# Kernel optimization log

Measured on AMD Instinct MI355X. Metric: run time of the kernel, lower is better.

Reference implementation:

```python
import jax, jax.numpy as jnp
import numpy as np

H_DIM = 1024
N_HEADS = 16
HEAD_D = H_DIM // N_HEADS  # 64


def setup_inputs() -> dict:
    key = jax.random.key(0)
    ks = jax.random.split(key, 10)
    B, T, C = 2, 2048, H_DIM
    init = 1.0 / np.sqrt(C)  # lecun_normal-scale stand-in
    src = jax.random.normal(ks[0], (B, T, C), dtype=jnp.float32)
    mask = jnp.ones((B, T), dtype=jnp.float32)  # unused when causal
    Wq = jax.random.normal(ks[1], (C, H_DIM), dtype=jnp.float32) * init
    Wk = jax.random.normal(ks[2], (C, H_DIM), dtype=jnp.float32) * init
    Wv = jax.random.normal(ks[3], (C, H_DIM), dtype=jnp.float32) * init
    Wo = jax.random.normal(ks[4], (H_DIM, H_DIM), dtype=jnp.float32) * init
    bq = jnp.zeros((H_DIM,), jnp.float32)
    bk = jnp.zeros((H_DIM,), jnp.float32)
    bv = jnp.zeros((H_DIM,), jnp.float32)
    bo = jnp.zeros((H_DIM,), jnp.float32)
    return {"src": src, "mask": mask, "Wq": Wq, "bq": bq, "Wk": Wk, "bk": bk,
            "Wv": Wv, "bv": bv, "Wo": Wo, "bo": bo}


def reference(src, mask, Wq, bq, Wk, bk, Wv, bv, Wo, bo):
    # MaskedCausalAttention forward, deterministic=True (dropout = identity),
    # use_causal_mask=True.
    B, T, C = src.shape
    N, D = N_HEADS, HEAD_D
    # q,k,v: [B, N, T, D]
    q = (src @ Wq + bq).reshape(B, T, N, D).transpose(0, 2, 1, 3)
    k = (src @ Wk + bk).reshape(B, T, N, D).transpose(0, 2, 1, 3)
    v = (src @ Wv + bv).reshape(B, T, N, D).transpose(0, 2, 1, 3)
    # scores: [B, N, T, T]
    scores = jnp.einsum('bntd,bnsd->bnts', q, k) / jnp.sqrt(jnp.float32(D))
    causal = jnp.tril(jnp.ones((T, T), dtype=bool))[None, None]
    scores = jnp.where(causal, scores, -jnp.inf)
    probs = jax.nn.softmax(scores, axis=-1)
    attn = jnp.einsum('bnts,bnsd->bntd', probs, v)  # [B, N, T, D]
    attn = attn.transpose(0, 2, 1, 3).reshape(B, T, N * D)
    return attn @ Wo + bo
```

## Files before the change

kernel.cpp:

```cpp
#include <hip/hip_runtime.h>
#include <hip/hip_bf16.h>

typedef __hip_bfloat16 bf16;
typedef __attribute__((ext_vector_type(8))) short short8;
typedef __attribute__((ext_vector_type(4))) float f32x4;

#define BATCH 2
#define SEQ   2048
#define HDIM  1024
#define NHEAD 16
#define DHEAD 64
#define MROWS (BATCH*SEQ)

#define QSCALE 0.18033688f
#define EXP2F(x) __builtin_amdgcn_exp2f(x)

static __device__ __forceinline__ short f2bs(float x) {
    __hip_bfloat16 h = (__hip_bfloat16)x;
    return *reinterpret_cast<short*>(&h);
}
static __device__ __forceinline__ unsigned int pk2(float a, float b) {
    __hip_bfloat162 h = __float22bfloat162_rn(make_float2(a, b));
    return *reinterpret_cast<unsigned int*>(&h);
}

static __device__ __forceinline__ void gload16(const void* g, void* l) {
    __builtin_amdgcn_global_load_lds(
        (const __attribute__((address_space(1))) unsigned int*)g,
        (__attribute__((address_space(3))) unsigned int*)l, 16, 0, 0);
}

__global__ __launch_bounds__(256) void prep1(const float* __restrict__ src,
        const float* __restrict__ Wq, const float* __restrict__ Wk,
        const float* __restrict__ Wv, const float* __restrict__ Wo,
        short* __restrict__ Sb, short* __restrict__ WT,
        short* __restrict__ WoT)
{
    __shared__ float t[64][65];
    const int bx = blockIdx.x, tid = threadIdx.x;
    if (bx < 4096) {
        int i = bx * 256 + tid;
        float4 v = ((const float4*)src)[i];
        ushort4 o;
        o.x = (unsigned short)f2bs(v.x);
        o.y = (unsigned short)f2bs(v.y);
        o.z = (unsigned short)f2bs(v.z);
        o.w = (unsigned short)f2bs(v.w);
        ((ushort4*)Sb)[i] = o;
        return;
    }
    const int tb = bx - 4096;
    const int wsel = tb >> 8;
    const float* W = (wsel == 0) ? Wq : (wsel == 1) ? Wk : (wsel == 2) ? Wv : Wo;
    short* dst = (wsel < 3) ? WT : WoT;
    const int roff = (wsel < 3) ? wsel * 1024 : 0;
    const int t8 = tb & 255;
    const int n0 = (t8 & 15) * 64, k0 = (t8 >> 4) * 64;
#pragma unroll
    for (int i = 0; i < 16; i++) {
        int idx = tid + i * 256, r = idx >> 6, c = idx & 63;
        t[r][c] = W[(size_t)(k0 + r) * HDIM + n0 + c];
    }
    __syncthreads();
#pragma unroll
    for (int i = 0; i < 16; i++) {
        int idx = tid + i * 256, c = idx >> 6, r = idx & 63;
        dst[(size_t)(roff + n0 + c) * HDIM + k0 + r] = f2bs(t[r][c]);
    }
}

__global__ __launch_bounds__(256) void gemm_qkv(const short* __restrict__ A,
        const short* __restrict__ Bt,
        const float* __restrict__ bq, const float* __restrict__ bk,
        const float* __restrict__ bv,
        short* __restrict__ Qout, short* __restrict__ Kout,
        short* __restrict__ Vtout)
{
    __shared__ short As[16 * 512];
    __shared__ short Bs[16 * 512];
    const int tid = threadIdx.x, lane = tid & 63, w = tid >> 6;
    const int quad = lane >> 4, l15 = lane & 15;
    const int m0 = blockIdx.y * 128, n0 = blockIdx.x * 128;
    const int wr = w >> 1, wc = w & 1;

    const short* gsrc[8];
    short* ldst[8];
#pragma unroll
    for (int i = 0; i < 8; i++) {
        int u = w * 8 + i;
        if (u < 16) {
            int mi = u >> 1, kh = u & 1;
            gsrc[i] = A + (size_t)(m0 + mi * 16 + l15) * HDIM + kh * 32 + quad * 8;
            ldst[i] = &As[u * 512];
        } else {
            int v = u - 16, ni = v >> 1, kh = v & 1;
            gsrc[i] = Bt + (size_t)(n0 + ni * 16 + l15) * HDIM + kh * 32 + quad * 8;
            ldst[i] = &Bs[v * 512];
        }
    }

    f32x4 acc[4][4];
#pragma unroll
    for (int i = 0; i < 4; i++)
#pragma unroll
        for (int j = 0; j < 4; j++) acc[i][j] = (f32x4){0.f, 0.f, 0.f, 0.f};

    for (int kk = 0; kk < 16; ++kk) {
        if (kk) __syncthreads();
#pragma unroll
        for (int i = 0; i < 8; i++) {
            gload16(gsrc[i], ldst[i]);
            gsrc[i] += 64;
        }
        __syncthreads();

#pragma unroll
        for (int kh = 0; kh < 2; kh++) {
            short8 af[4], bfr[4];
#pragma unroll
            for (int mi = 0; mi < 4; mi++)
                af[mi] = *(const short8*)&As[((wr * 4 + mi) * 2 + kh) * 512 + lane * 8];
#pragma unroll
            for (int ni = 0; ni < 4; ni++)
                bfr[ni] = *(const short8*)&Bs[((wc * 4 + ni) * 2 + kh) * 512 + lane * 8];
#pragma unroll
            for (int mi = 0; mi < 4; mi++)
#pragma unroll
                for (int ni = 0; ni < 4; ni++)
                    acc[mi][ni] = __builtin_amdgcn_mfma_f32_16x16x32_bf16(
                                      af[mi], bfr[ni], acc[mi][ni], 0, 0, 0);
        }
    }

    const int region = n0 >> 10;
    if (region < 2) {
        const float* bias = region ? bk : bq;
        const float oscale = region ? 1.0f : QSCALE;
        short* C = region ? Kout : Qout;
#pragma unroll
        for (int mi = 0; mi < 4; mi++) {
            int mB = m0 + (wr * 4 + mi) * 16 + quad * 4;
#pragma unroll
            for (int ni = 0; ni < 4; ni++) {
                int nl = (n0 + (wc * 4 + ni) * 16 + l15) & 1023;
                float bb = bias[nl];
#pragma unroll
                for (int r = 0; r < 4; r++)
                    C[(size_t)(mB + r) * HDIM + nl] =
                        f2bs((acc[mi][ni][r] + bb) * oscale);
            }
        }
    } else {
#pragma unroll
        for (int mi = 0; mi < 4; mi++) {
            int mB = m0 + (wr * 4 + mi) * 16 + quad * 4;
            int bb = mB >> 11, t = mB & 2047;
#pragma unroll
            for (int ni = 0; ni < 4; ni++) {
                int n = n0 + (wc * 4 + ni) * 16 + l15;
                int h = (n >> 6) & 15, d = n & 63;
                float bvv = bv[n & 1023];
                size_t base = ((size_t)((bb * NHEAD + h) * DHEAD + d)) * SEQ + t;
                ushort4 pk;
                pk.x = (unsigned short)f2bs(acc[mi][ni][0] + bvv);
                pk.y = (unsigned short)f2bs(acc[mi][ni][1] + bvv);
                pk.z = (unsigned short)f2bs(acc[mi][ni][2] + bvv);
                pk.w = (unsigned short)f2bs(acc[mi][ni][3] + bvv);
                *(ushort4*)(Vtout + base) = pk;
            }
        }
    }
}

__global__ __launch_bounds__(256) void attn_mfma(const short* __restrict__ Qb,
        const short* __restrict__ Kb, const short* __restrict__ Vt,
        short* __restrict__ Ab)
{
    __shared__ short SMEM[20992];
    const int tid = threadIdx.x, lane = tid & 63, w = tid >> 6;
    const int quad = lane >> 4, l15 = lane & 15;
    const int L = blockIdx.x;

    const int pair = (L & 7) + 8 * ((L >> 3) & 3);
    const int strip = 31 - (L >> 5);
    const int b = pair >> 4, head = pair & 15;

    const short* Kbh = Kb + (size_t)b * SEQ * HDIM + head * DHEAD;
    const short* Vth = Vt + (size_t)(b * NHEAD + head) * DHEAD * SEQ;
    short* Pw = SMEM + 16384 + w * 1152;

    const int qbase = strip * 64;
    const int qr = qbase + w * 16 + l15;

    const short* qptr = Qb + (size_t)(b * SEQ + qr) * HDIM + head * DHEAD + quad * 8;
    short8 bq0 = *(const short8*)qptr;
    short8 bq1 = *(const short8*)(qptr + 32);

    const short* gp[4];
    int stp[4], ldo[4];
#pragma unroll
    for (int i = 0; i < 4; i++) {
        int u = w * 4 + i;
        if (u < 8) {
            int t = u >> 1, h = u & 1;
            gp[i] = Kbh + (size_t)(t * 16 + l15) * HDIM + h * 32 + quad * 8;
            stp[i] = 64 * HDIM;
        } else {
            int c = u - 8, dt = c >> 1, kh = c & 1;
            gp[i] = Vth + (size_t)(dt * 16 + l15) * SEQ + kh * 32 + quad * 8;
            stp[i] = 64;
        }
        ldo[i] = u * 512;
    }

    f32x4 o[4];
#pragma unroll
    for (int dt = 0; dt < 4; dt++) o[dt] = (f32x4){0.f, 0.f, 0.f, 0.f};
    float psum = 0.f;

#pragma unroll
    for (int i = 0; i < 4; i++) { gload16(gp[i], &SMEM[ldo[i]]); gp[i] += stp[i]; }

    for (int it = 0; it <= strip; ++it) {
        const int cur = it & 1;
        short* Ks = &SMEM[cur * 8192];
        short* Vs = Ks + 4096;

        if (it < strip) {
            short* nb = &SMEM[(cur ^ 1) * 8192];
#pragma unroll
            for (int i = 0; i < 4; i++) { gload16(gp[i], nb + ldo[i]); gp[i] += stp[i]; }
            asm volatile("s_waitcnt vmcnt(4)" ::: "memory");
        } else {
            asm volatile("s_waitcnt vmcnt(0)" ::: "memory");
        }
        __builtin_amdgcn_s_barrier();
        const int s0 = it * 64;
        f32x4 sv[4];
        __builtin_amdgcn_s_setprio(1);
#pragma unroll
        for (int t = 0; t < 4; t++) {
            sv[t] = (f32x4){0.f, 0.f, 0.f, 0.f};
            short8 k0 = *(const short8*)&Ks[(t * 2) * 512 + lane * 8];
            short8 k1 = *(const short8*)&Ks[(t * 2 + 1) * 512 + lane * 8];
            sv[t] = __builtin_amdgcn_mfma_f32_16x16x32_bf16(k0, bq0, sv[t], 0, 0, 0);
            sv[t] = __builtin_amdgcn_mfma_f32_16x16x32_bf16(k1, bq1, sv[t], 0, 0, 0);
        }
        __builtin_amdgcn_s_setprio(0);

        float p[16];
        if (it == strip) {
#pragma unroll
            for (int t = 0; t < 4; t++)
#pragma unroll
                for (int r = 0; r < 4; r++) {
                    int key = s0 + t * 16 + quad * 4 + r;
                    p[t * 4 + r] = (key <= qr) ? EXP2F(sv[t][r]) : 0.f;
                }
        } else {
#pragma unroll
            for (int t = 0; t < 4; t++)
#pragma unroll
                for (int r = 0; r < 4; r++)
                    p[t * 4 + r] = EXP2F(sv[t][r]);
        }
#pragma unroll
        for (int i = 0; i < 16; i++) psum += p[i];

#pragma unroll
        for (int t = 0; t < 4; t++) {
            uint2 u2;
            u2.x = pk2(p[t * 4],     p[t * 4 + 1]);
            u2.y = pk2(p[t * 4 + 2], p[t * 4 + 3]);
            *(uint2*)&Pw[l15 * 72 + t * 16 + quad * 4] = u2;
        }
        short8 bp0 = *(const short8*)&Pw[l15 * 72 + quad * 8];
        short8 bp1 = *(const short8*)&Pw[l15 * 72 + 32 + quad * 8];

        __builtin_amdgcn_s_setprio(1);
#pragma unroll
        for (int dt = 0; dt < 4; dt++) {
            short8 av0 = *(const short8*)&Vs[(dt * 2) * 512 + lane * 8];
            short8 av1 = *(const short8*)&Vs[(dt * 2 + 1) * 512 + lane * 8];
            o[dt] = __builtin_amdgcn_mfma_f32_16x16x32_bf16(av0, bp0, o[dt], 0, 0, 0);
            o[dt] = __builtin_amdgcn_mfma_f32_16x16x32_bf16(av1, bp1, o[dt], 0, 0, 0);
        }
        __builtin_amdgcn_s_setprio(0);
        __builtin_amdgcn_s_barrier();
    }

    float lrow = psum + __shfl_xor(psum, 16);
    lrow += __shfl_xor(lrow, 32);
    const float inv = 1.f / lrow;

    const size_t obase = (size_t)(b * SEQ + qr) * HDIM + head * DHEAD;
#pragma unroll
    for (int dt = 0; dt < 4; dt++) {
        uint2 u2;
        u2.x = pk2(o[dt][0] * inv, o[dt][1] * inv);
        u2.y = pk2(o[dt][2] * inv, o[dt][3] * inv);
        *(uint2*)&Ab[obase + dt * 16 + quad * 4] = u2;
    }
}

__global__ __launch_bounds__(256) void gemm_o(const short* __restrict__ A,
        const short* __restrict__ Bt, const float* __restrict__ bo,
        float* __restrict__ Out)
{
    __shared__ short As[8 * 512];
    __shared__ short Bs[16 * 512];
    const int tid = threadIdx.x, lane = tid & 63, w = tid >> 6;
    const int quad = lane >> 4, l15 = lane & 15;
    const int m0 = blockIdx.y * 64, n0 = blockIdx.x * 128;
    const int wr = w >> 1, wc = w & 1;

    const short* gsrc[6];
    short* ldst[6];
#pragma unroll
    for (int i = 0; i < 6; i++) {
        int u = w * 6 + i;
        if (u < 8) {
            int mi = u >> 1, kh = u & 1;
            gsrc[i] = A + (size_t)(m0 + mi * 16 + l15) * HDIM + kh * 32 + quad * 8;
            ldst[i] = &As[u * 512];
        } else {
            int v = u - 8, ni = v >> 1, kh = v & 1;
            gsrc[i] = Bt + (size_t)(n0 + ni * 16 + l15) * HDIM + kh * 32 + quad * 8;
            ldst[i] = &Bs[v * 512];
        }
    }

    f32x4 acc[2][4];
#pragma unroll
    for (int i = 0; i < 2; i++)
#pragma unroll
        for (int j = 0; j < 4; j++) acc[i][j] = (f32x4){0.f, 0.f, 0.f, 0.f};

    for (int kk = 0; kk < 16; ++kk) {
        if (kk) __syncthreads();
#pragma unroll
        for (int i = 0; i < 6; i++) {
            gload16(gsrc[i], ldst[i]);
            gsrc[i] += 64;
        }
        __syncthreads();

#pragma unroll
        for (int kh = 0; kh < 2; kh++) {
            short8 af[2], bfr[4];
#pragma unroll
            for (int mi = 0; mi < 2; mi++)
                af[mi] = *(const short8*)&As[((wr * 2 + mi) * 2 + kh) * 512 + lane * 8];
#pragma unroll
            for (int ni = 0; ni < 4; ni++)
                bfr[ni] = *(const short8*)&Bs[((wc * 4 + ni) * 2 + kh) * 512 + lane * 8];
#pragma unroll
            for (int mi = 0; mi < 2; mi++)
#pragma unroll
                for (int ni = 0; ni < 4; ni++)
                    acc[mi][ni] = __builtin_amdgcn_mfma_f32_16x16x32_bf16(
                                      af[mi], bfr[ni], acc[mi][ni], 0, 0, 0);
        }
    }

#pragma unroll
    for (int mi = 0; mi < 2; mi++) {
        int mB = m0 + (wr * 2 + mi) * 16 + quad * 4;
#pragma unroll
        for (int ni = 0; ni < 4; ni++) {
            int n = n0 + (wc * 4 + ni) * 16 + l15;
            float bb = bo[n];
#pragma unroll
            for (int r = 0; r < 4; r++)
                Out[(size_t)(mB + r) * HDIM + n] = acc[mi][ni][r] + bb;
        }
    }
}

extern "C" void kernel_launch(void* const* d_in, const int* in_sizes, int n_in,
                              void* d_out, int out_size, void* d_ws, size_t ws_size,
                              hipStream_t stream)
{
    const float* src = (const float*)d_in[0];
    const float* Wq = (const float*)d_in[2];
    const float* bq = (const float*)d_in[3];
    const float* Wk = (const float*)d_in[4];
    const float* bk = (const float*)d_in[5];
    const float* Wv = (const float*)d_in[6];
    const float* bv = (const float*)d_in[7];
    const float* Wo = (const float*)d_in[8];
    const float* bo = (const float*)d_in[9];
    float* out = (float*)d_out;

    short* Sb   = (short*)d_ws;
    short* Qb   = Sb + (size_t)MROWS * HDIM;
    short* Kb   = Qb + (size_t)MROWS * HDIM;
    short* Vt   = Kb + (size_t)MROWS * HDIM;
    short* WoT  = Vt + (size_t)MROWS * HDIM;
    short* WT   = (short*)d_out;
    short* Ab   = Qb;

    dim3 blk(256);

    prep1<<<dim3(4096 + 1024), blk, 0, stream>>>(src, Wq, Wk, Wv, Wo, Sb, WT, WoT);

    gemm_qkv<<<dim3(24, 32), blk, 0, stream>>>(Sb, WT, bq, bk, bv, Qb, Kb, Vt);

    attn_mfma<<<dim3(1024), blk, 0, stream>>>(Qb, Kb, Vt, Ab);

    gemm_o<<<dim3(8, 64), blk, 0, stream>>>(Ab, WoT, bo, out);
}
```

Before: 224.7 us.

## Double-buffer LDS tiles in QKV and output GEMMs with async prefetch

Both GEMM kernels now keep two LDS stages and issue the global-to-LDS loads for the next k-tile before computing on the current one. Explicit vmcnt waits and raw s_barrier calls replace the two __syncthreads per iteration, so load latency can overlap the MFMA work. This doubles LDS use per block, which may lower occupancy. Correctness relies on the hand-written waitcnt values matching the outstanding load count and on the barrier not waiting for LDS reads.

Measured after the change: 210.8 us. 6.2% less time.

```diff
diff --git a/kernel.cpp b/kernel.cpp
--- a/kernel.cpp
+++ b/kernel.cpp
@@ -76,8 +76,7 @@
         short* __restrict__ Qout, short* __restrict__ Kout,
         short* __restrict__ Vtout)
 {
-    __shared__ short As[16 * 512];
-    __shared__ short Bs[16 * 512];
+    __shared__ short SM[2 * 16384];
     const int tid = threadIdx.x, lane = tid & 63, w = tid >> 6;
     const int quad = lane >> 4, l15 = lane & 15;
     const int m0 = blockIdx.y * 128, n0 = blockIdx.x * 128;
@@ -91,11 +90,11 @@
         if (u < 16) {
             int mi = u >> 1, kh = u & 1;
             gsrc[i] = A + (size_t)(m0 + mi * 16 + l15) * HDIM + kh * 32 + quad * 8;
-            ldst[i] = &As[u * 512];
+            ldst[i] = &SM[u * 512];
         } else {
             int v = u - 16, ni = v >> 1, kh = v & 1;
             gsrc[i] = Bt + (size_t)(n0 + ni * 16 + l15) * HDIM + kh * 32 + quad * 8;
-            ldst[i] = &Bs[v * 512];
+            ldst[i] = &SM[8192 + v * 512];
         }
     }
 
@@ -105,24 +104,31 @@
 #pragma unroll
         for (int j = 0; j < 4; j++) acc[i][j] = (f32x4){0.f, 0.f, 0.f, 0.f};
 
+#pragma unroll
+    for (int i = 0; i < 8; i++) { gload16(gsrc[i], ldst[i]); gsrc[i] += 64; }
+
     for (int kk = 0; kk < 16; ++kk) {
-        if (kk) __syncthreads();
-#pragma unroll
-        for (int i = 0; i < 8; i++) {
-            gload16(gsrc[i], ldst[i]);
-            gsrc[i] += 64;
-        }
-        __syncthreads();
-
+        const int cur = kk & 1;
+        if (kk < 15) {
+            const int nb = (cur ^ 1) << 14;
+#pragma unroll
+            for (int i = 0; i < 8; i++) { gload16(gsrc[i], ldst[i] + nb); gsrc[i] += 64; }
+            asm volatile("s_waitcnt vmcnt(8)" ::: "memory");
+        } else {
+            asm volatile("s_waitcnt vmcnt(0)" ::: "memory");
+        }
+        __builtin_amdgcn_s_barrier();
+        const short* Asb = &SM[cur << 14];
+        const short* Bsb = Asb + 8192;
 #pragma unroll
         for (int kh = 0; kh < 2; kh++) {
             short8 af[4], bfr[4];
 #pragma unroll
             for (int mi = 0; mi < 4; mi++)
-                af[mi] = *(const short8*)&As[((wr * 4 + mi) * 2 + kh) * 512 + lane * 8];
+                af[mi] = *(const short8*)&Asb[((wr * 4 + mi) * 2 + kh) * 512 + lane * 8];
 #pragma unroll
             for (int ni = 0; ni < 4; ni++)
-                bfr[ni] = *(const short8*)&Bs[((wc * 4 + ni) * 2 + kh) * 512 + lane * 8];
+                bfr[ni] = *(const short8*)&Bsb[((wc * 4 + ni) * 2 + kh) * 512 + lane * 8];
 #pragma unroll
             for (int mi = 0; mi < 4; mi++)
 #pragma unroll
@@ -130,6 +136,7 @@
                     acc[mi][ni] = __builtin_amdgcn_mfma_f32_16x16x32_bf16(
                                       af[mi], bfr[ni], acc[mi][ni], 0, 0, 0);
         }
+        __builtin_amdgcn_s_barrier();
     }
 
     const int region = n0 >> 10;
@@ -307,8 +314,7 @@
         const short* __restrict__ Bt, const float* __restrict__ bo,
         float* __restrict__ Out)
 {
-    __shared__ short As[8 * 512];
-    __shared__ short Bs[16 * 512];
+    __shared__ short SM[2 * 12288];
     const int tid = threadIdx.x, lane = tid & 63, w = tid >> 6;
     const int quad = lane >> 4, l15 = lane & 15;
     const int m0 = blockIdx.y * 64, n0 = blockIdx.x * 128;
@@ -322,11 +328,11 @@
         if (u < 8) {
             int mi = u >> 1, kh = u & 1;
             gsrc[i] = A + (size_t)(m0 + mi * 16 + l15) * HDIM + kh * 32 + quad * 8;
-            ldst[i] = &As[u * 512];
+            ldst[i] = &SM[u * 512];
         } else {
             int v = u - 8, ni = v >> 1, kh = v & 1;
             gsrc[i] = Bt + (size_t)(n0 + ni * 16 + l15) * HDIM + kh * 32 + quad * 8;
-            ldst[i] = &Bs[v * 512];
+            ldst[i] = &SM[4096 + v * 512];
         }
     }
 
@@ -336,24 +342,32 @@
 #pragma unroll
         for (int j = 0; j < 4; j++) acc[i][j] = (f32x4){0.f, 0.f, 0.f, 0.f};
 
+#pragma unroll
+    for (int i = 0; i < 6; i++) { gload16(gsrc[i], ldst[i]); gsrc[i] += 64; }
+
     for (int kk = 0; kk < 16; ++kk) {
-        if (kk) __syncthreads();
-#pragma unroll
-        for (int i = 0; i < 6; i++) {
-            gload16(gsrc[i], ldst[i]);
-            gsrc[i] += 64;
-        }
-        __syncthreads();
-
+        const int cur = kk & 1;
+        if (kk < 15) {
+            const int nb = (cur ^ 1) * 12288;
+#pragma unroll
+            for (int i = 0; i < 6; i++) { gload16(gsrc[i], ldst[i] + nb); gsrc[i] += 64; }
+            asm volatile("s_waitcnt vmcnt(6)" ::: "memory");
+        } else {
+            asm volatile("s_waitcnt vmcnt(0)" ::: "memory");
+        }
+        __builtin_amdgcn_s_barrier();
+
+        const short* Asb = &SM[cur * 12288];
+        const short* Bsb = Asb + 4096;
 #pragma unroll
         for (int kh = 0; kh < 2; kh++) {
             short8 af[2], bfr[4];
 #pragma unroll
             for (int mi = 0; mi < 2; mi++)
-                af[mi] = *(const short8*)&As[((wr * 2 + mi) * 2 + kh) * 512 + lane * 8];
+                af[mi] = *(const short8*)&Asb[((wr * 2 + mi) * 2 + kh) * 512 + lane * 8];
 #pragma unroll
             for (int ni = 0; ni < 4; ni++)
-                bfr[ni] = *(const short8*)&Bs[((wc * 4 + ni) * 2 + kh) * 512 + lane * 8];
+                bfr[ni] = *(const short8*)&Bsb[((wc * 4 + ni) * 2 + kh) * 512 + lane * 8];
 #pragma unroll
             for (int mi = 0; mi < 2; mi++)
 #pragma unroll
@@ -361,6 +375,7 @@
                     acc[mi][ni] = __builtin_amdgcn_mfma_f32_16x16x32_bf16(
                                       af[mi], bfr[ni], acc[mi][ni], 0, 0, 0);
         }
+        __builtin_amdgcn_s_barrier();
     }
 
 #pragma unroll
```

## Load GEMM fragments directly from global memory into registers with double buffering

Applied to the files above, without the earlier changes.

Both projection GEMMs stop staging tiles in LDS with global-to-LDS loads and barriers. Each wave now loads its MFMA A/B fragments straight from global memory into registers, using a two-stage register double buffer to overlap loads with MFMAs, and the launch bounds ask for two blocks per CU. This removes LDS traffic and __syncthreads, but tiles shared between waves are now loaded redundantly from global/L2, and the 16-byte row-strided fragment loads are less coalesced.

New measurement: 296.3 us. +31.9%, slower.

```diff
diff --git a/kernel.cpp b/kernel.cpp
--- a/kernel.cpp
+++ b/kernel.cpp
@@ -69,35 +69,26 @@
     }
 }
 
-__global__ __launch_bounds__(256) void gemm_qkv(const short* __restrict__ A,
+__global__ __launch_bounds__(256, 2) void gemm_qkv(const short* __restrict__ A,
         const short* __restrict__ Bt,
         const float* __restrict__ bq, const float* __restrict__ bk,
         const float* __restrict__ bv,
         short* __restrict__ Qout, short* __restrict__ Kout,
         short* __restrict__ Vtout)
 {
-    __shared__ short As[16 * 512];
-    __shared__ short Bs[16 * 512];
     const int tid = threadIdx.x, lane = tid & 63, w = tid >> 6;
     const int quad = lane >> 4, l15 = lane & 15;
     const int m0 = blockIdx.y * 128, n0 = blockIdx.x * 128;
     const int wr = w >> 1, wc = w & 1;
 
-    const short* gsrc[8];
-    short* ldst[8];
-#pragma unroll
-    for (int i = 0; i < 8; i++) {
-        int u = w * 8 + i;
-        if (u < 16) {
-            int mi = u >> 1, kh = u & 1;
-            gsrc[i] = A + (size_t)(m0 + mi * 16 + l15) * HDIM + kh * 32 + quad * 8;
-            ldst[i] = &As[u * 512];
-        } else {
-            int v = u - 16, ni = v >> 1, kh = v & 1;
-            gsrc[i] = Bt + (size_t)(n0 + ni * 16 + l15) * HDIM + kh * 32 + quad * 8;
-            ldst[i] = &Bs[v * 512];
-        }
-    }
+    const short* ap[4];
+    const short* bp[4];
+#pragma unroll
+    for (int mi = 0; mi < 4; mi++)
+        ap[mi] = A + (size_t)(m0 + wr * 64 + mi * 16 + l15) * HDIM + quad * 8;
+#pragma unroll
+    for (int ni = 0; ni < 4; ni++)
+        bp[ni] = Bt + (size_t)(n0 + wc * 64 + ni * 16 + l15) * HDIM + quad * 8;
 
     f32x4 acc[4][4];
 #pragma unroll
@@ -105,31 +96,35 @@
 #pragma unroll
         for (int j = 0; j < 4; j++) acc[i][j] = (f32x4){0.f, 0.f, 0.f, 0.f};
 
-    for (int kk = 0; kk < 16; ++kk) {
-        if (kk) __syncthreads();
-#pragma unroll
-        for (int i = 0; i < 8; i++) {
-            gload16(gsrc[i], ldst[i]);
-            gsrc[i] += 64;
-        }
-        __syncthreads();
-
-#pragma unroll
-        for (int kh = 0; kh < 2; kh++) {
-            short8 af[4], bfr[4];
-#pragma unroll
-            for (int mi = 0; mi < 4; mi++)
-                af[mi] = *(const short8*)&As[((wr * 4 + mi) * 2 + kh) * 512 + lane * 8];
+    short8 a0[4], b0[4], a1[4], b1[4];
+#pragma unroll
+    for (int mi = 0; mi < 4; mi++) { a0[mi] = *(const short8*)ap[mi]; ap[mi] += 32; }
+#pragma unroll
+    for (int ni = 0; ni < 4; ni++) { b0[ni] = *(const short8*)bp[ni]; bp[ni] += 32; }
+
+    for (int kk = 0; kk < 32; kk += 2) {
+#pragma unroll
+        for (int mi = 0; mi < 4; mi++) { a1[mi] = *(const short8*)ap[mi]; ap[mi] += 32; }
+#pragma unroll
+        for (int ni = 0; ni < 4; ni++) { b1[ni] = *(const short8*)bp[ni]; bp[ni] += 32; }
+#pragma unroll
+        for (int mi = 0; mi < 4; mi++)
 #pragma unroll
             for (int ni = 0; ni < 4; ni++)
-                bfr[ni] = *(const short8*)&Bs[((wc * 4 + ni) * 2 + kh) * 512 + lane * 8];
-#pragma unroll
-            for (int mi = 0; mi < 4; mi++)
-#pragma unroll
-                for (int ni = 0; ni < 4; ni++)
-                    acc[mi][ni] = __builtin_amdgcn_mfma_f32_16x16x32_bf16(
-                                      af[mi], bfr[ni], acc[mi][ni], 0, 0, 0);
-        }
+                acc[mi][ni] = __builtin_amdgcn_mfma_f32_16x16x32_bf16(
+                                  a0[mi], b0[ni], acc[mi][ni], 0, 0, 0);
+        if (kk < 30) {
+#pragma unroll
+            for (int mi = 0; mi < 4; mi++) { a0[mi] = *(const short8*)ap[mi]; ap[mi] += 32; }
+#pragma unroll
+            for (int ni = 0; ni < 4; ni++) { b0[ni] = *(const short8*)bp[ni]; bp[ni] += 32; }
+        }
+#pragma unroll
+        for (int mi = 0; mi < 4; mi++)
+#pragma unroll
+            for (int ni = 0; ni < 4; ni++)
+                acc[mi][ni] = __builtin_amdgcn_mfma_f32_16x16x32_bf16(
+                                  a1[mi], b1[ni], acc[mi][ni], 0, 0, 0);
     }
 
     const int region = n0 >> 10;
@@ -303,32 +298,23 @@
     }
 }
 
-__global__ __launch_bounds__(256) void gemm_o(const short* __restrict__ A,
+__global__ __launch_bounds__(256, 2) void gemm_o(const short* __restrict__ A,
         const short* __restrict__ Bt, const float* __restrict__ bo,
         float* __restrict__ Out)
 {
-    __shared__ short As[8 * 512];
-    __shared__ short Bs[16 * 512];
     const int tid = threadIdx.x, lane = tid & 63, w = tid >> 6;
     const int quad = lane >> 4, l15 = lane & 15;
     const int m0 = blockIdx.y * 64, n0 = blockIdx.x * 128;
     const int wr = w >> 1, wc = w & 1;
 
-    const short* gsrc[6];
-    short* ldst[6];
-#pragma unroll
-    for (int i = 0; i < 6; i++) {
-        int u = w * 6 + i;
-        if (u < 8) {
-            int mi = u >> 1, kh = u & 1;
-            gsrc[i] = A + (size_t)(m0 + mi * 16 + l15) * HDIM + kh * 32 + quad * 8;
-            ldst[i] = &As[u * 512];
-        } else {
-            int v = u - 8, ni = v >> 1, kh = v & 1;
-            gsrc[i] = Bt + (size_t)(n0 + ni * 16 + l15) * HDIM + kh * 32 + quad * 8;
-            ldst[i] = &Bs[v * 512];
-        }
-    }
+    const short* ap[2];
+    const short* bp[4];
+#pragma unroll
+    for (int mi = 0; mi < 2; mi++)
+        ap[mi] = A + (size_t)(m0 + wr * 32 + mi * 16 + l15) * HDIM + quad * 8;
+#pragma unroll
+    for (int ni = 0; ni < 4; ni++)
+        bp[ni] = Bt + (size_t)(n0 + wc * 64 + ni * 16 + l15) * HDIM + quad * 8;
 
     f32x4 acc[2][4];
 #pragma unroll
@@ -336,31 +322,35 @@
 #pragma unroll
         for (int j = 0; j < 4; j++) acc[i][j] = (f32x4){0.f, 0.f, 0.f, 0.f};
 
-    for (int kk = 0; kk < 16; ++kk) {
-        if (kk) __syncthreads();
-#pragma unroll
-        for (int i = 0; i < 6; i++) {
-            gload16(gsrc[i], ldst[i]);
-            gsrc[i] += 64;
-        }
-        __syncthreads();
-
-#pragma unroll
-        for (int kh = 0; kh < 2; kh++) {
-            short8 af[2], bfr[4];
-#pragma unroll
-            for (int mi = 0; mi < 2; mi++)
-                af[mi] = *(const short8*)&As[((wr * 2 + mi) * 2 + kh) * 512 + lane * 8];
+    short8 a0[2], b0[4], a1[2], b1[4];
+#pragma unroll
+    for (int mi = 0; mi < 2; mi++) { a0[mi] = *(const short8*)ap[mi]; ap[mi] += 32; }
+#pragma unroll
+    for (int ni = 0; ni < 4; ni++) { b0[ni] = *(const short8*)bp[ni]; bp[ni] += 32; }
+
+    for (int kk = 0; kk < 32; kk += 2) {
+#pragma unroll
+        for (int mi = 0; mi < 2; mi++) { a1[mi] = *(const short8*)ap[mi]; ap[mi] += 32; }
+#pragma unroll
+        for (int ni = 0; ni < 4; ni++) { b1[ni] = *(const short8*)bp[ni]; bp[ni] += 32; }
+#pragma unroll
+        for (int mi = 0; mi < 2; mi++)
 #pragma unroll
             for (int ni = 0; ni < 4; ni++)
-                bfr[ni] = *(const short8*)&Bs[((wc * 4 + ni) * 2 + kh) * 512 + lane * 8];
-#pragma unroll
-            for (int mi = 0; mi < 2; mi++)
-#pragma unroll
-                for (int ni = 0; ni < 4; ni++)
-                    acc[mi][ni] = __builtin_amdgcn_mfma_f32_16x16x32_bf16(
-                                      af[mi], bfr[ni], acc[mi][ni], 0, 0, 0);
-        }
+                acc[mi][ni] = __builtin_amdgcn_mfma_f32_16x16x32_bf16(
+                                  a0[mi], b0[ni], acc[mi][ni], 0, 0, 0);
+        if (kk < 30) {
+#pragma unroll
+            for (int mi = 0; mi < 2; mi++) { a0[mi] = *(const short8*)ap[mi]; ap[mi] += 32; }
+#pragma unroll
+            for (int ni = 0; ni < 4; ni++) { b0[ni] = *(const short8*)bp[ni]; bp[ni] += 32; }
+        }
+#pragma unroll
+        for (int mi = 0; mi < 2; mi++)
+#pragma unroll
+            for (int ni = 0; ni < 4; ni++)
+                acc[mi][ni] = __builtin_amdgcn_mfma_f32_16x16x32_bf16(
+                                  a1[mi], b1[ni], acc[mi][ni], 0, 0, 0);
     }
 
 #pragma unroll
```
